# Optimization experiments

Hardware: AMD Instinct MI355X
Metric: run time of the kernel (lower is better)

Reference implementation:

```python
import jax, jax.numpy as jnp
import numpy as np

WS = 16  # window_size

def _conv1x1(x, w, b):
    # x: [n,c,h,w], w: [out,in], b: [out]
    return jnp.einsum('nchw,oc->nohw', x, w) + b[None, :, None, None]

def _se_attention(x, w1, b1, w2, b2):
    # global avg pool -> conv -> relu -> conv -> sigmoid; returns [n,C,1,1]
    p = x.mean(axis=(2, 3), keepdims=True)
    h = jax.nn.relu(_conv1x1(p, w1, b1))
    return jax.nn.sigmoid(_conv1x1(h, w2, b2))

def setup_inputs() -> dict:
    key = jax.random.key(0)
    ks = jax.random.split(key, 13)
    B, C, H, W = 8, 96, 256, 256
    Cr = C // 3
    s = 0.02
    return {
        'x': jax.random.normal(ks[0], (B, C, H, W), jnp.float32),
        'w_real': jax.random.normal(ks[1], (C, C), jnp.float32) * s,
        'b_real': jnp.zeros((C,), jnp.float32),
        'w_imag': jax.random.normal(ks[2], (C, C), jnp.float32) * s,
        'b_imag': jnp.zeros((C,), jnp.float32),
        'car_w1': jax.random.normal(ks[3], (Cr, C), jnp.float32) * s,
        'car_b1': jnp.zeros((Cr,), jnp.float32),
        'car_w2': jax.random.normal(ks[4], (C, Cr), jnp.float32) * s,
        'car_b2': jnp.zeros((C,), jnp.float32),
        'cai_w1': jax.random.normal(ks[5], (Cr, C), jnp.float32) * s,
        'cai_b1': jnp.zeros((Cr,), jnp.float32),
        'cai_w2': jax.random.normal(ks[6], (C, Cr), jnp.float32) * s,
        'cai_b2': jnp.zeros((C,), jnp.float32),
    }

def reference(x, w_real, b_real, w_imag, b_imag,
              car_w1, car_b1, car_w2, car_b2,
              cai_w1, cai_b1, cai_w2, cai_b2):
    B, C, H, W = x.shape
    nH, nW = H // WS, W // WS
    # window partition: [B,C,H,W] -> [B*nH*nW, C, WS, WS]
    xw = x.reshape(B, C, nH, WS, nW, WS)
    xw = xw.transpose(0, 2, 4, 1, 3, 5).reshape(-1, C, WS, WS)
    # 2D FFT per window, ortho norm
    x_fft = jnp.fft.fft2(xw, norm='ortho')
    real_conv = _conv1x1(jnp.real(x_fft), w_real, b_real)
    imag_conv = _conv1x1(jnp.imag(x_fft), w_imag, b_imag)
    real_att = _se_attention(real_conv, car_w1, car_b1, car_w2, car_b2)
    imag_att = _se_attention(imag_conv, cai_w1, cai_b1, cai_w2, cai_b2)
    real_conv = real_conv * (1.0 + real_att)
    imag_conv = imag_conv * (1.0 + imag_att)
    x_fft_enh = jax.lax.complex(real_conv, imag_conv)
    x_ifft = jnp.real(jnp.fft.ifft2(x_fft_enh, norm='ortho'))
    # window merge: [B*nH*nW, C, WS, WS] -> [B,C,H,W]
    out = x_ifft.reshape(B, nH, nW, C, WS, WS)
    out = out.transpose(0, 3, 1, 4, 2, 5).reshape(B, C, H, W)
    return out
```

## Files before the change

### kernel.cpp

```cpp
#include <hip/hip_runtime.h>
#include <hip/hip_bf16.h>
#include <math.h>

#define NWIN 2048

typedef __bf16 v8bf __attribute__((ext_vector_type(8)));
typedef __bf16 v2bf __attribute__((ext_vector_type(2)));
typedef float  v4f  __attribute__((ext_vector_type(4)));

__global__ __launch_bounds__(128) void se_alpha_kernel(
    const float* __restrict__ x,
    const float* __restrict__ w_real, const float* __restrict__ b_real,
    const float* __restrict__ car_w1, const float* __restrict__ car_b1,
    const float* __restrict__ car_w2, const float* __restrict__ car_b2,
    const float* __restrict__ b_imag,
    const float* __restrict__ cai_w1, const float* __restrict__ cai_b1,
    const float* __restrict__ cai_w2, const float* __restrict__ cai_b2,
    float* __restrict__ alpha, float* __restrict__ beta)
{
    __shared__ float wr_s[96 * 97];
    __shared__ float vec_s[96];
    __shared__ float pr_s[96];
    __shared__ float h1_s[32];
    const int t = threadIdx.x;
    const int n = blockIdx.x;

    if (n < NWIN) {
        const int b = n >> 8, wh = (n >> 4) & 15, ww = n & 15;
        for (int idx = t; idx < 96 * 96; idx += 128) {
            int o = idx / 96;
            int c = idx - o * 96;
            wr_s[o * 97 + c] = w_real[idx];
        }
        if (t < 96)
            vec_s[t] = x[(((size_t)(b * 96 + t)) * 256 + wh * 16) * 256 + ww * 16];
        __syncthreads();
        if (t < 96) {
            float acc = 0.f;
            #pragma unroll 8
            for (int c = 0; c < 96; ++c) acc += wr_s[t * 97 + c] * vec_s[c];
            pr_s[t] = acc * (1.0f / 16.0f) + b_real[t];
        }
        __syncthreads();
        if (t < 32) {
            float acc = car_b1[t];
            for (int o = 0; o < 96; ++o) acc += car_w1[t * 96 + o] * pr_s[o];
            h1_s[t] = fmaxf(acc, 0.f);
        }
        __syncthreads();
        if (t < 96) {
            float acc = car_b2[t];
            for (int j = 0; j < 32; ++j) acc += car_w2[t * 32 + j] * h1_s[j];
            alpha[n * 96 + t] = 1.f + 1.f / (1.f + __expf(-acc));
        }
    } else {
        if (t < 32) {
            float acc = cai_b1[t];
            for (int o = 0; o < 96; ++o) acc += cai_w1[t * 96 + o] * b_imag[o];
            h1_s[t] = fmaxf(acc, 0.f);
        }
        __syncthreads();
        if (t < 96) {
            float acc = cai_b2[t];
            for (int j = 0; j < 32; ++j) acc += cai_w2[t * 32 + j] * h1_s[j];
            beta[t] = 1.f + 1.f / (1.f + __expf(-acc));
        }
    }
}

__global__ __launch_bounds__(256, 2) void wfca_main_kernel(
    const float* __restrict__ x,
    const float* __restrict__ w_real, const float* __restrict__ w_imag,
    const float* __restrict__ b_real,
    const float* __restrict__ alpha, const float* __restrict__ beta,
    float* __restrict__ out)
{
    __shared__ __bf16 x_lds[256 * 40];
    __shared__ __bf16 w1_lds[96 * 40];
    __shared__ __bf16 w2_lds[96 * 40];

    const int t = threadIdx.x;
    const int nwin = blockIdx.x;
    const int b = nwin >> 8, wh = (nwin >> 4) & 15, ww = nwin & 15;
    const int lane = t & 63;
    const int wave = t >> 6;
    const int l16 = lane & 15;
    const int quad = lane >> 4;

    const int sw = t & 15;
    const int scp = t >> 4;
    const int wc = t & 31;
    const int wo0 = t >> 5;

    v4f acc[4][6];
    #pragma unroll
    for (int i = 0; i < 4; ++i)
        #pragma unroll
        for (int j = 0; j < 6; ++j)
            acc[i][j] = v4f{0.f, 0.f, 0.f, 0.f};

    const size_t xbase = (((size_t)b * 96) * 256 + wh * 16) * 256 + ww * 16;

    for (int kc = 0; kc < 3; ++kc) {
        const int c0 = kc * 32;
        if (kc) __syncthreads();

        {
            const float* xp = x + xbase + (size_t)(c0 + 2 * scp) * 65536 + sw;
            #pragma unroll
            for (int h = 0; h < 16; ++h) {
                float f0 = xp[h * 256];
                float f1 = xp[h * 256 + 65536];
                v2bf pk;
                pk[0] = (__bf16)f0;
                pk[1] = (__bf16)f1;
                *(v2bf*)&x_lds[(h * 16 + sw) * 40 + 2 * scp] = pk;
            }
        }
        {
            #pragma unroll
            for (int i = 0; i < 12; ++i) {
                int o = wo0 + 8 * i;
                float wr = w_real[o * 96 + c0 + wc];
                float wi = w_imag[o * 96 + c0 + wc];
                float a  = alpha[nwin * 96 + o];
                float bt = beta[o];
                w1_lds[o * 40 + wc] = (__bf16)(0.5f * (a * wr + bt * wi));
                w2_lds[o * 40 + wc] = (__bf16)(0.5f * (a * wr - bt * wi));
            }
        }
        __syncthreads();

        v8bf a_x[4], a_f[4];
        #pragma unroll
        for (int mi = 0; mi < 4; ++mi) {
            int h = wave * 4 + mi;
            a_x[mi] = *(const v8bf*)&x_lds[(h * 16 + l16) * 40 + quad * 8];
            int hf = (16 - h) & 15;
            int wf = (16 - l16) & 15;
            a_f[mi] = *(const v8bf*)&x_lds[(hf * 16 + wf) * 40 + quad * 8];
        }
        #pragma unroll
        for (int n = 0; n < 6; ++n) {
            v8bf b1 = *(const v8bf*)&w1_lds[(n * 16 + l16) * 40 + quad * 8];
            v8bf b2 = *(const v8bf*)&w2_lds[(n * 16 + l16) * 40 + quad * 8];
            #pragma unroll
            for (int mi = 0; mi < 4; ++mi) {
                acc[mi][n] = __builtin_amdgcn_mfma_f32_16x16x32_bf16(a_x[mi], b1, acc[mi][n], 0, 0, 0);
                acc[mi][n] = __builtin_amdgcn_mfma_f32_16x16x32_bf16(a_f[mi], b2, acc[mi][n], 0, 0, 0);
            }
        }
    }

    #pragma unroll
    for (int n = 0; n < 6; ++n) {
        int o = n * 16 + l16;
        #pragma unroll
        for (int mi = 0; mi < 4; ++mi) {
            int h = wave * 4 + mi;
            v4f v = acc[mi][n];
            if (h == 0 && quad == 0) {
                v[0] += 16.f * alpha[nwin * 96 + o] * b_real[o];
            }
            size_t idx = (((size_t)(b * 96 + o)) * 256 + wh * 16 + h) * 256 + ww * 16 + quad * 4;
            *(v4f*)(out + idx) = v;
        }
    }
}

extern "C" void kernel_launch(void* const* d_in, const int* in_sizes, int n_in,
                              void* d_out, int out_size, void* d_ws, size_t ws_size,
                              hipStream_t stream) {
    const float* x      = (const float*)d_in[0];
    const float* w_real = (const float*)d_in[1];
    const float* b_real = (const float*)d_in[2];
    const float* w_imag = (const float*)d_in[3];
    const float* b_imag = (const float*)d_in[4];
    const float* car_w1 = (const float*)d_in[5];
    const float* car_b1 = (const float*)d_in[6];
    const float* car_w2 = (const float*)d_in[7];
    const float* car_b2 = (const float*)d_in[8];
    const float* cai_w1 = (const float*)d_in[9];
    const float* cai_b1 = (const float*)d_in[10];
    const float* cai_w2 = (const float*)d_in[11];
    const float* cai_b2 = (const float*)d_in[12];
    float* out = (float*)d_out;

    float* alpha = (float*)d_ws;
    float* beta  = alpha + NWIN * 96;

    se_alpha_kernel<<<NWIN + 1, 128, 0, stream>>>(
        x, w_real, b_real, car_w1, car_b1, car_w2, car_b2,
        b_imag, cai_w1, cai_b1, cai_w2, cai_b2, alpha, beta);

    wfca_main_kernel<<<NWIN, 256, 0, stream>>>(
        x, w_real, w_imag, b_real, alpha, beta, out);
}
```

Baseline: 430.8 us.

## Batch 16 windows per SE block and raise main kernel occupancy to 4 waves

The SE alpha kernel now processes 16 windows per 256-thread block, so the 96x96 w_real load into LDS is amortized over 16 windows instead of repeated 2048 times. The main kernel's launch bound goes from 2 to 4 blocks per CU, and its MFMA loop is reordered so A fragments are loaded per row tile inside the loop. This lowers register pressure enough to fit the higher occupancy. The cost is more repeated LDS reads of the B fragments, and a possible risk of register spills under the tighter bound.

```diff
diff --git a/kernel.cpp b/kernel.cpp
--- a/kernel.cpp
+++ b/kernel.cpp
@@ -8,7 +8,7 @@
 typedef __bf16 v2bf __attribute__((ext_vector_type(2)));
 typedef float  v4f  __attribute__((ext_vector_type(4)));
 
-__global__ __launch_bounds__(128) void se_alpha_kernel(
+__global__ __launch_bounds__(256) void se_alpha_kernel(
     const float* __restrict__ x,
     const float* __restrict__ w_real, const float* __restrict__ b_real,
     const float* __restrict__ car_w1, const float* __restrict__ car_b1,
@@ -19,56 +19,72 @@
     float* __restrict__ alpha, float* __restrict__ beta)
 {
     __shared__ float wr_s[96 * 97];
-    __shared__ float vec_s[96];
-    __shared__ float pr_s[96];
-    __shared__ float h1_s[32];
+    __shared__ float corner_s[16][100];
+    __shared__ float p_s[16][100];
+    __shared__ float h1_s[16][32];
     const int t = threadIdx.x;
-    const int n = blockIdx.x;
-
-    if (n < NWIN) {
-        const int b = n >> 8, wh = (n >> 4) & 15, ww = n & 15;
-        for (int idx = t; idx < 96 * 96; idx += 128) {
-            int o = idx / 96;
-            int c = idx - o * 96;
+    const int blk = blockIdx.x;
+
+    if (blk < 128) {
+        const int n0 = blk * 16;
+        for (int idx = t; idx < 96 * 96; idx += 256) {
+            int o = idx / 96, c = idx - o * 96;
             wr_s[o * 97 + c] = w_real[idx];
         }
-        if (t < 96)
-            vec_s[t] = x[(((size_t)(b * 96 + t)) * 256 + wh * 16) * 256 + ww * 16];
-        __syncthreads();
-        if (t < 96) {
+        #pragma unroll
+        for (int i = 0; i < 6; ++i) {
+            int idx = t + 256 * i;
+            int wl = idx / 96, c = idx - wl * 96;
+            int n = n0 + wl;
+            int b = n >> 8, wh = (n >> 4) & 15, ww = n & 15;
+            corner_s[wl][c] = x[(((size_t)(b * 96 + c)) * 256 + wh * 16) * 256 + ww * 16];
+        }
+        __syncthreads();
+        #pragma unroll
+        for (int i = 0; i < 6; ++i) {
+            int idx = t + 256 * i;
+            int wl = idx / 96, o = idx - wl * 96;
             float acc = 0.f;
             #pragma unroll 8
-            for (int c = 0; c < 96; ++c) acc += wr_s[t * 97 + c] * vec_s[c];
-            pr_s[t] = acc * (1.0f / 16.0f) + b_real[t];
-        }
-        __syncthreads();
-        if (t < 32) {
-            float acc = car_b1[t];
-            for (int o = 0; o < 96; ++o) acc += car_w1[t * 96 + o] * pr_s[o];
-            h1_s[t] = fmaxf(acc, 0.f);
-        }
-        __syncthreads();
-        if (t < 96) {
-            float acc = car_b2[t];
-            for (int j = 0; j < 32; ++j) acc += car_w2[t * 32 + j] * h1_s[j];
-            alpha[n * 96 + t] = 1.f + 1.f / (1.f + __expf(-acc));
+            for (int c = 0; c < 96; ++c) acc += wr_s[o * 97 + c] * corner_s[wl][c];
+            p_s[wl][o] = acc * (1.0f / 16.0f) + b_real[o];
+        }
+        __syncthreads();
+        #pragma unroll
+        for (int i = 0; i < 2; ++i) {
+            int idx = t + 256 * i;
+            int wl = idx >> 5, j = idx & 31;
+            float acc = car_b1[j];
+            #pragma unroll 8
+            for (int o = 0; o < 96; ++o) acc += car_w1[j * 96 + o] * p_s[wl][o];
+            h1_s[wl][j] = fmaxf(acc, 0.f);
+        }
+        __syncthreads();
+        #pragma unroll
+        for (int i = 0; i < 6; ++i) {
+            int idx = t + 256 * i;
+            int wl = idx / 96, o = idx - wl * 96;
+            float acc = car_b2[o];
+            #pragma unroll
+            for (int j = 0; j < 32; ++j) acc += car_w2[o * 32 + j] * h1_s[wl][j];
+            alpha[(n0 + wl) * 96 + o] = 1.f + 1.f / (1.f + __expf(-acc));
         }
     } else {
         if (t < 32) {
             float acc = cai_b1[t];
             for (int o = 0; o < 96; ++o) acc += cai_w1[t * 96 + o] * b_imag[o];
-            h1_s[t] = fmaxf(acc, 0.f);
+            h1_s[0][t] = fmaxf(acc, 0.f);
         }
         __syncthreads();
         if (t < 96) {
             float acc = cai_b2[t];
-            for (int j = 0; j < 32; ++j) acc += cai_w2[t * 32 + j] * h1_s[j];
+            for (int j = 0; j < 32; ++j) acc += cai_w2[t * 32 + j] * h1_s[0][j];
             beta[t] = 1.f + 1.f / (1.f + __expf(-acc));
         }
     }
 }
 
-__global__ __launch_bounds__(256, 2) void wfca_main_kernel(
+__global__ __launch_bounds__(256, 4) void wfca_main_kernel(
     const float* __restrict__ x,
     const float* __restrict__ w_real, const float* __restrict__ w_imag,
     const float* __restrict__ b_real,
@@ -131,23 +147,19 @@
         }
         __syncthreads();
 
-        v8bf a_x[4], a_f[4];
         #pragma unroll
         for (int mi = 0; mi < 4; ++mi) {
             int h = wave * 4 + mi;
-            a_x[mi] = *(const v8bf*)&x_lds[(h * 16 + l16) * 40 + quad * 8];
+            v8bf a_x = *(const v8bf*)&x_lds[(h * 16 + l16) * 40 + quad * 8];
             int hf = (16 - h) & 15;
             int wf = (16 - l16) & 15;
-            a_f[mi] = *(const v8bf*)&x_lds[(hf * 16 + wf) * 40 + quad * 8];
-        }
-        #pragma unroll
-        for (int n = 0; n < 6; ++n) {
-            v8bf b1 = *(const v8bf*)&w1_lds[(n * 16 + l16) * 40 + quad * 8];
-            v8bf b2 = *(const v8bf*)&w2_lds[(n * 16 + l16) * 40 + quad * 8];
-            #pragma unroll
-            for (int mi = 0; mi < 4; ++mi) {
-                acc[mi][n] = __builtin_amdgcn_mfma_f32_16x16x32_bf16(a_x[mi], b1, acc[mi][n], 0, 0, 0);
-                acc[mi][n] = __builtin_amdgcn_mfma_f32_16x16x32_bf16(a_f[mi], b2, acc[mi][n], 0, 0, 0);
+            v8bf a_f = *(const v8bf*)&x_lds[(hf * 16 + wf) * 40 + quad * 8];
+            #pragma unroll
+            for (int n = 0; n < 6; ++n) {
+                v8bf b1 = *(const v8bf*)&w1_lds[(n * 16 + l16) * 40 + quad * 8];
+                v8bf b2 = *(const v8bf*)&w2_lds[(n * 16 + l16) * 40 + quad * 8];
+                acc[mi][n] = __builtin_amdgcn_mfma_f32_16x16x32_bf16(a_x, b1, acc[mi][n], 0, 0, 0);
+                acc[mi][n] = __builtin_amdgcn_mfma_f32_16x16x32_bf16(a_f, b2, acc[mi][n], 0, 0, 0);
             }
         }
     }
@@ -189,7 +201,7 @@
     float* alpha = (float*)d_ws;
     float* beta  = alpha + NWIN * 96;
 
-    se_alpha_kernel<<<NWIN + 1, 128, 0, stream>>>(
+    se_alpha_kernel<<<129, 256, 0, stream>>>(
         x, w_real, b_real, car_w1, car_b1, car_w2, car_b2,
         b_imag, cai_w1, cai_b1, cai_w2, cai_b2, alpha, beta);
 
```

Result: slower. 629.1 us (+46.0%).
